# Performance work log

Hardware: AMD Instinct MI355X
Metric: run time of the kernel (lower is better)

## Reference

```python
import jax, jax.numpy as jnp
import numpy as np

B, L, D, H, W = 2, 4096, 1024, 16, 128
E = D // H

def _ln(x, g, b):
    m = jnp.mean(x, axis=-1, keepdims=True)
    v = jnp.mean((x - m) ** 2, axis=-1, keepdims=True)
    return (x - m) / jnp.sqrt(v + 1e-5) * g + b

def _swa(xn, Wqkv, bqkv, Wp, bp):
    # causal sliding-window attention: query i attends keys j in [i-W+1, i]
    b_, l_, d_ = xn.shape
    nb = l_ // W
    qkv = xn @ Wqkv + bqkv
    q, k, v = jnp.split(qkv, 3, axis=-1)
    def heads(t):
        return t.reshape(b_, l_, H, E).transpose(0, 2, 1, 3)  # [B,H,L,E]
    q, k, v = heads(q), heads(k), heads(v)
    def blk(t):
        return t.reshape(b_, H, nb, W, E)
    qb, kb, vb = blk(q), blk(k), blk(v)
    # each query block sees previous block + own block (covers the W-band)
    kprev = jnp.pad(kb, ((0, 0), (0, 0), (1, 0), (0, 0), (0, 0)))[:, :, :nb]
    vprev = jnp.pad(vb, ((0, 0), (0, 0), (1, 0), (0, 0), (0, 0)))[:, :, :nb]
    kc = jnp.concatenate([kprev, kb], axis=3)  # [B,H,nb,2W,E]
    vc = jnp.concatenate([vprev, vb], axis=3)
    scores = jnp.einsum('bhnre,bhnse->bhnrs', qb, kc) / np.float32(np.sqrt(E))
    r = jnp.arange(W)[:, None]
    s = jnp.arange(2 * W)[None, :]
    band = (s >= r + 1) & (s <= r + W)          # local coords of [i-W+1, i]
    first = band & (s >= W)                     # block 0 has no previous block
    mask = jnp.concatenate([first[None], jnp.broadcast_to(band, (nb - 1, W, 2 * W))], axis=0)
    scores = jnp.where(mask[None, None], scores, jnp.float32(-1e30))
    attn = jax.nn.softmax(scores, axis=-1)
    out = jnp.einsum('bhnrs,bhnse->bhnre', attn, vc)
    out = out.reshape(b_, H, l_, E).transpose(0, 2, 1, 3).reshape(b_, l_, d_)
    return out @ Wp + bp

def _linattn(xn, Wqkv, bqkv, Wo, bo):
    # chunked recurrent form of causal linear attention (same math as cumsum version)
    b_, l_, d_ = xn.shape
    C = 128
    nc = l_ // C
    qkv = xn @ Wqkv + bqkv
    q, k, v = jnp.split(qkv, 3, axis=-1)
    q = q.reshape(b_, l_, H, E)
    k = k.reshape(b_, l_, H, E)
    v = v.reshape(b_, l_, H, E)
    q = jax.nn.elu(q * np.float32(E ** -0.5)) + np.float32(1.0001)
    k = jax.nn.elu(k) + np.float32(1.0001)
    def chunks(t):
        return t.reshape(b_, nc, C, H, E).transpose(1, 0, 3, 2, 4)  # [nc,B,H,C,E]
    qc, kc, vc = chunks(q), chunks(k), chunks(v)
    tril = jnp.tril(jnp.ones((C, C), jnp.float32))
    def step(carry, inp):
        S, z = carry
        qi, ki, vi = inp
        A = jnp.einsum('bhce,bhde->bhcd', qi, ki) * tril
        num = jnp.einsum('bhce,bhef->bhcf', qi, S) + jnp.einsum('bhcd,bhdf->bhcf', A, vi)
        den = jnp.einsum('bhce,bhe->bhc', qi, z) + A.sum(-1)
        o = num / (den[..., None] + 1e-6)
        S = S + jnp.einsum('bhce,bhcf->bhef', ki, vi)
        z = z + ki.sum(2)
        return (S, z), o
    S0 = jnp.zeros((b_, H, E, E), jnp.float32)
    z0 = jnp.zeros((b_, H, E), jnp.float32)
    _, out = jax.lax.scan(step, (S0, z0), (qc, kc, vc))
    out = out.transpose(1, 0, 3, 2, 4).reshape(b_, l_, d_)
    return out @ Wo + bo

def setup_inputs() -> dict:
    key = jax.random.key(0)
    ks = jax.random.split(key, 9)
    def w(k, shape, s=0.02):
        return jax.random.normal(k, shape, jnp.float32) * s
    return {
        'x': jax.random.normal(ks[0], (B, L, D), jnp.float32),
        'g1': jnp.ones((D,), jnp.float32), 'b1': jnp.zeros((D,), jnp.float32),
        'Wqkv_a': w(ks[1], (D, 3 * D)), 'bqkv_a': jnp.zeros((3 * D,), jnp.float32),
        'Wp_a': w(ks[2], (D, D)), 'bp_a': jnp.zeros((D,), jnp.float32),
        'Wqkv_s': w(ks[3], (D, 3 * D)), 'bqkv_s': jnp.zeros((3 * D,), jnp.float32),
        'Wo_s': w(ks[4], (D, D)), 'bo_s': jnp.zeros((D,), jnp.float32),
        'Wo': w(ks[5], (D, D)), 'bo': jnp.zeros((D,), jnp.float32),
        'gm': jnp.ones((D,), jnp.float32), 'bm': jnp.zeros((D,), jnp.float32),
        'W1': w(ks[6], (D, 4 * D)), 'b1m': jnp.zeros((4 * D,), jnp.float32),
        'W2': w(ks[7], (4 * D, D)), 'b2m': jnp.zeros((D,), jnp.float32),
    }

def reference(x, g1, b1, Wqkv_a, bqkv_a, Wp_a, bp_a, Wqkv_s, bqkv_s, Wo_s, bo_s,
              Wo, bo, gm, bm, W1, b1m, W2, b2m):
    xn = _ln(x, g1, b1)
    attn_out = _swa(xn, Wqkv_a, bqkv_a, Wp_a, bp_a)
    ssm_out = _linattn(xn, Wqkv_s, bqkv_s, Wo_s, bo_s)
    mixed = (attn_out + ssm_out) @ Wo + bo
    x1 = x + mixed
    h = _ln(x1, gm, bm)
    mlp = jax.nn.gelu(h @ W1 + b1m, approximate=False) @ W2 + b2m
    return x1 + mlp
```

## Files before the change

### kernel.cpp

```cpp
#include <hip/hip_runtime.h>
#include <hip/hip_bf16.h>
#include <math.h>

typedef __hip_bfloat16 bf16;
typedef float f32x4 __attribute__((ext_vector_type(4)));
typedef short short8 __attribute__((ext_vector_type(8)));
typedef unsigned short u16x4 __attribute__((ext_vector_type(4)));
typedef unsigned short u16x8 __attribute__((ext_vector_type(8)));

#define AS1 __attribute__((address_space(1)))
#define AS3 __attribute__((address_space(3)))

__device__ __forceinline__ void gload16(const void* g, void* l) {
  __builtin_amdgcn_global_load_lds((const AS1 unsigned int*)g, (AS3 unsigned int*)l, 16, 0, 0);
}
__device__ __forceinline__ float b2f(unsigned short u) {
  union { unsigned int i; float f; } c; c.i = ((unsigned int)u) << 16; return c.f;
}
__device__ __forceinline__ unsigned short f2b(float f) {
  bf16 h = __float2bfloat16(f);
  unsigned short s; __builtin_memcpy(&s, &h, 2); return s;
}
__device__ __forceinline__ f32x4 mfma16(short8 a, short8 b, f32x4 c) {
  return __builtin_amdgcn_mfma_f32_16x16x32_bf16(a, b, c, 0, 0, 0);
}

#define BARR asm volatile("s_barrier" ::: "memory")
#define LGKM0 asm volatile("s_waitcnt lgkmcnt(0)" ::: "memory")
#define VM8 asm volatile("s_waitcnt vmcnt(8)" ::: "memory")
#define VM6 asm volatile("s_waitcnt vmcnt(6)" ::: "memory")
#define VM4 asm volatile("s_waitcnt vmcnt(4)" ::: "memory")
#define VM3 asm volatile("s_waitcnt vmcnt(3)" ::: "memory")
#define VM0 asm volatile("s_waitcnt vmcnt(0)" ::: "memory")
#define SB0 __builtin_amdgcn_sched_barrier(0)
#define PRIO1 __builtin_amdgcn_s_setprio(1)
#define PRIO0 __builtin_amdgcn_s_setprio(0)

__global__ __launch_bounds__(256) void ln_kernel(
    const float* __restrict__ X, const float* __restrict__ G,
    const float* __restrict__ Bb, unsigned short* __restrict__ Y) {
  __shared__ float red[8];
  const size_t row = blockIdx.x;
  const int tid = threadIdx.x;
  f32x4 v = *(const f32x4*)&X[row * 1024 + tid * 4];
  float s = 0.f, sq = 0.f;
#pragma unroll
  for (int j = 0; j < 4; ++j) { s += v[j]; sq += v[j] * v[j]; }
#pragma unroll
  for (int o = 1; o < 64; o <<= 1) { s += __shfl_xor(s, o); sq += __shfl_xor(sq, o); }
  if ((tid & 63) == 0) { red[tid >> 6] = s; red[4 + (tid >> 6)] = sq; }
  __syncthreads();
  s = red[0] + red[1] + red[2] + red[3];
  sq = red[4] + red[5] + red[6] + red[7];
  const float mean = s * (1.f / 1024.f);
  const float var = sq * (1.f / 1024.f) - mean * mean;
  const float inv = 1.f / sqrtf(var + 1e-5f);
  f32x4 gv = *(const f32x4*)&G[tid * 4];
  f32x4 bv = *(const f32x4*)&Bb[tid * 4];
  u16x4 ov;
#pragma unroll
  for (int j = 0; j < 4; ++j) ov[j] = f2b((v[j] - mean) * inv * gv[j] + bv[j]);
  *(u16x4*)&Y[row * 1024 + tid * 4] = ov;
}

struct TW7 {
  const float* S[7];
  unsigned short* D[7];
  int N[7], dld[7], doff[7], gx[7];
  int start[8];
};
__global__ __launch_bounds__(256) void transpose_w7(TW7 tw) {
  __shared__ __attribute__((aligned(16))) unsigned short t[64][72];
  const int bid = blockIdx.x;
  int c = 0;
#pragma unroll
  for (int j = 0; j < 7; ++j)
    if (bid >= tw.start[j]) c = j;
  const int local = bid - tw.start[c];
  const int k0 = (local % tw.gx[c]) * 64, n0 = (local / tw.gx[c]) * 64;
  const float* S = tw.S[c];
  unsigned short* D = tw.D[c];
  const int N = tw.N[c], dld = tw.dld[c], doff = tw.doff[c];
  const int tid = threadIdx.x;
#pragma unroll
  for (int i = 0; i < 2; ++i) {
    int cc = i * 256 + tid;
    int row = cc >> 3, c8 = cc & 7;
    f32x4 a = *(const f32x4*)&S[(size_t)(k0 + row) * N + n0 + c8 * 8];
    f32x4 b = *(const f32x4*)&S[(size_t)(k0 + row) * N + n0 + c8 * 8 + 4];
    u16x8 o;
#pragma unroll
    for (int j = 0; j < 4; ++j) { o[j] = f2b(a[j]); o[4 + j] = f2b(b[j]); }
    *(u16x8*)&t[row][c8 * 8] = o;
  }
  __syncthreads();
#pragma unroll
  for (int i = 0; i < 2; ++i) {
    int cc = i * 256 + tid;
    int nrow = cc >> 3, k8 = cc & 7;
    u16x8 o;
#pragma unroll
    for (int j = 0; j < 8; ++j) o[j] = t[k8 * 8 + j][nrow];
    *(u16x8*)&D[(size_t)(n0 + nrow) * dld + doff + k0 + k8 * 8] = o;
  }
}

__global__ __launch_bounds__(256) void bias_comb(
    const float* __restrict__ a, const float* __restrict__ b, float* __restrict__ o) {
  int i = blockIdx.x * 256 + threadIdx.x;
  o[i] = a[i] + b[i];
}

__global__ __launch_bounds__(256) void bias_cat(
    const float* __restrict__ a, const float* __restrict__ b, float* __restrict__ o, int N) {
  int i = blockIdx.x * 256 + threadIdx.x;
  o[i] = (i < N) ? a[i] : b[i - N];
}

#define EPI_STORE 0
#define EPI_GELU 1
#define EPI_RES 2

template <int EPI, int OF32>
__global__ __launch_bounds__(512, 2) void gemm_big(
    const unsigned short* __restrict__ A, const unsigned short* __restrict__ Bt,
    const float* __restrict__ bias, void* __restrict__ Cv,
    const float* __restrict__ res, int K, int ldA, int ldC) {
  __shared__ __attribute__((aligned(16))) unsigned short Abuf[2][2][16 * 512];
  __shared__ __attribute__((aligned(16))) unsigned short Bbuf[2][2][16 * 512];
  const int tid = threadIdx.x, lane = tid & 63, wv = tid >> 6;
  const int g = lane >> 4, r = lane & 15;
  const int wr = wv >> 2, wc = wv & 3;
  const size_t arow0 = (size_t)blockIdx.x * 256;
  const size_t brow0 = (size_t)blockIdx.y * 256;
  const size_t ldAs = (size_t)ldA, Ksz = (size_t)K;
  const unsigned short* gA0 = A + (arow0 + (size_t)((2 * wv + 0) * 16 + r)) * ldAs + g * 8;
  const unsigned short* gA1 = A + (arow0 + (size_t)((2 * wv + 1) * 16 + r)) * ldAs + g * 8;
  const unsigned short* gB0 = Bt + (brow0 + (size_t)((2 * wv + 0) * 16 + r)) * Ksz + g * 8;
  const unsigned short* gB1 = Bt + (brow0 + (size_t)((2 * wv + 1) * 16 + r)) * Ksz + g * 8;
  const int nT = K >> 6;
  f32x4 acc[8][4] = {};
  short8 af[8], bfr[4];

#define STG(BUF, KK, T_) do { size_t o_ = (size_t)(T_) * 64 + (KK) * 32;            \
    gload16(gA0 + o_, &Abuf[BUF][KK][(2 * wv + 0) * 512]);                           \
    gload16(gA1 + o_, &Abuf[BUF][KK][(2 * wv + 1) * 512]);                           \
    gload16(gB0 + o_, &Bbuf[BUF][KK][(2 * wv + 0) * 512]);                           \
    gload16(gB1 + o_, &Bbuf[BUF][KK][(2 * wv + 1) * 512]); } while (0)
#define RDF(CUR, KK) do {                                                            \
    _Pragma("unroll") for (int m_ = 0; m_ < 8; ++m_)                                 \
      af[m_] = *(const short8*)&Abuf[CUR][KK][(wr * 8 + m_) * 512 + lane * 8];       \
    _Pragma("unroll") for (int n_ = 0; n_ < 4; ++n_)                                 \
      bfr[n_] = *(const short8*)&Bbuf[CUR][KK][(wc * 4 + n_) * 512 + lane * 8]; } while (0)
#define MMQ() _Pragma("unroll") for (int m_ = 0; m_ < 8; ++m_)                       \
    _Pragma("unroll") for (int n_ = 0; n_ < 4; ++n_)                                 \
      acc[m_][n_] = mfma16(af[m_], bfr[n_], acc[m_][n_]);

  STG(0, 0, 0); STG(0, 1, 0); STG(1, 0, 1);
  VM8; BARR; SB0;

  for (int T = 0; T < nT; ++T) {
    const int cur = T & 1;
    RDF(cur, 0);
    if (T + 1 < nT) STG(cur ^ 1, 1, T + 1);
    BARR; LGKM0; SB0;
    PRIO1; MMQ(); PRIO0;
    if (T + 1 < nT) { VM8; } else { VM0; }
    BARR; SB0;
    RDF(cur, 1);
    if (T + 2 < nT) STG(cur, 0, T + 2);
    BARR; LGKM0; SB0;
    PRIO1; MMQ(); PRIO0;
    if (T + 2 < nT) { VM8; } else if (T + 1 < nT) { VM4; }
    BARR; SB0;
  }
#undef STG
#undef RDF
#undef MMQ

#pragma unroll
  for (int m = 0; m < 8; ++m) {
#pragma unroll
    for (int n = 0; n < 4; ++n) {
      const int col = (int)brow0 + wc * 64 + n * 16 + r;
      const float bv = bias[col];
#pragma unroll
      for (int i = 0; i < 4; ++i) {
        const size_t row = arow0 + wr * 128 + m * 16 + g * 4 + i;
        float v = acc[m][n][i] + bv;
        if (EPI == EPI_GELU) v = 0.5f * v * (1.f + erff(v * 0.70710678118f));
        if (EPI == EPI_RES) v += res[row * ldC + col];
        if (OF32) ((float*)Cv)[row * ldC + col] = v;
        else ((unsigned short*)Cv)[row * ldC + col] = f2b(v);
      }
    }
  }
}

template <int EPI, int OF32>
__global__ __launch_bounds__(512, 2) void gemm_sml(
    const unsigned short* __restrict__ A, const unsigned short* __restrict__ Bt,
    const float* __restrict__ bias, void* __restrict__ Cv,
    const float* __restrict__ res, int K, int ldA, int ldC) {
  __shared__ __attribute__((aligned(16))) unsigned short Abuf[2][2][8 * 512];
  __shared__ __attribute__((aligned(16))) unsigned short Bbuf[2][2][16 * 512];
  const int tid = threadIdx.x, lane = tid & 63, wv = tid >> 6;
  const int g = lane >> 4, r = lane & 15;
  const int wr = wv >> 2, wc = wv & 3;
  const size_t arow0 = (size_t)blockIdx.x * 128;
  const size_t brow0 = (size_t)blockIdx.y * 256;
  const size_t ldAs = (size_t)ldA, Ksz = (size_t)K;
  const unsigned short* gAs = A + (arow0 + (size_t)(wv * 16 + r)) * ldAs + g * 8;
  const unsigned short* gB0 = Bt + (brow0 + (size_t)((2 * wv + 0) * 16 + r)) * Ksz + g * 8;
  const unsigned short* gB1 = Bt + (brow0 + (size_t)((2 * wv + 1) * 16 + r)) * Ksz + g * 8;
  const int nT = K >> 6;
  f32x4 acc[4][4] = {};
  short8 af[4], bfr[4];

#define STG(BUF, KK, T_) do { size_t o_ = (size_t)(T_) * 64 + (KK) * 32;            \
    gload16(gAs + o_, &Abuf[BUF][KK][wv * 512]);                                     \
    gload16(gB0 + o_, &Bbuf[BUF][KK][(2 * wv + 0) * 512]);                           \
    gload16(gB1 + o_, &Bbuf[BUF][KK][(2 * wv + 1) * 512]); } while (0)
#define RDF(CUR, KK) do {                                                            \
    _Pragma("unroll") for (int m_ = 0; m_ < 4; ++m_)                                 \
      af[m_] = *(const short8*)&Abuf[CUR][KK][(wr * 4 + m_) * 512 + lane * 8];       \
    _Pragma("unroll") for (int n_ = 0; n_ < 4; ++n_)                                 \
      bfr[n_] = *(const short8*)&Bbuf[CUR][KK][(wc * 4 + n_) * 512 + lane * 8]; } while (0)
#define MMQ() _Pragma("unroll") for (int m_ = 0; m_ < 4; ++m_)                       \
    _Pragma("unroll") for (int n_ = 0; n_ < 4; ++n_)                                 \
      acc[m_][n_] = mfma16(af[m_], bfr[n_], acc[m_][n_]);

  STG(0, 0, 0); STG(0, 1, 0); STG(1, 0, 1);
  VM6; BARR; SB0;

  for (int T = 0; T < nT; ++T) {
    const int cur = T & 1;
    RDF(cur, 0);
    if (T + 1 < nT) STG(cur ^ 1, 1, T + 1);
    BARR; LGKM0; SB0;
    PRIO1; MMQ(); PRIO0;
    if (T + 1 < nT) { VM6; } else { VM0; }
    BARR; SB0;
    RDF(cur, 1);
    if (T + 2 < nT) STG(cur, 0, T + 2);
    BARR; LGKM0; SB0;
    PRIO1; MMQ(); PRIO0;
    if (T + 2 < nT) { VM6; } else if (T + 1 < nT) { VM3; }
    BARR; SB0;
  }
#undef STG
#undef RDF
#undef MMQ

#pragma unroll
  for (int m = 0; m < 4; ++m) {
#pragma unroll
    for (int n = 0; n < 4; ++n) {
      const int col = (int)brow0 + wc * 64 + n * 16 + r;
      const float bv = bias[col];
#pragma unroll
      for (int i = 0; i < 4; ++i) {
        const size_t row = arow0 + wr * 64 + m * 16 + g * 4 + i;
        float v = acc[m][n][i] + bv;
        if (EPI == EPI_GELU) v = 0.5f * v * (1.f + erff(v * 0.70710678118f));
        if (EPI == EPI_RES) v += res[row * ldC + col];
        if (OF32) ((float*)Cv)[row * ldC + col] = v;
        else ((unsigned short*)Cv)[row * ldC + col] = f2b(v);
      }
    }
  }
}

__global__ __launch_bounds__(256) void swa_kernel(
    const unsigned short* __restrict__ qkv, unsigned short* __restrict__ outc) {
  __shared__ __attribute__((aligned(16))) unsigned short Ks[256 * 64];
  __shared__ __attribute__((aligned(16))) unsigned short Vt[64 * 264];
  __shared__ __attribute__((aligned(16))) unsigned short Ps[128 * 264];
  __shared__ __attribute__((aligned(16))) float dn[128];
  const int bid = blockIdx.x;
  const int qb = bid & 31, h = (bid >> 5) & 15, b = bid >> 9;
  const long btok = (long)b * 4096;
  const long tok0 = btok + (long)qb * 128;
  const int tid = threadIdx.x, lane = tid & 63, wv = tid >> 6;
  const int g = lane >> 4, r = lane & 15;

#pragma unroll
  for (int i = 0; i < 8; ++i) {
    int chunk = (wv * 8 + i) * 64 + lane;
    int s = chunk >> 3, cc = (chunk & 7) ^ (s & 7);
    long kt = tok0 - 128 + s; if (kt < btok) kt = btok;
    gload16(&qkv[(size_t)kt * 6144 + 1024 + h * 64 + cc * 8], &Ks[(wv * 8 + i) * 512]);
  }
#pragma unroll
  for (int i = 0; i < 8; ++i) {
    int chunk = i * 256 + tid;
    int s = chunk >> 3, e8 = chunk & 7;
    long kt = tok0 - 128 + s; if (kt < btok) kt = btok;
    u16x8 u = *(const u16x8*)&qkv[(size_t)kt * 6144 + 2048 + h * 64 + e8 * 8];
#pragma unroll
    for (int j = 0; j < 8; ++j) Vt[(e8 * 8 + j) * 264 + s] = u[j];
  }
  short8 qf[2][2];
#pragma unroll
  for (int m = 0; m < 2; ++m)
#pragma unroll
    for (int kc = 0; kc < 2; ++kc)
      qf[m][kc] = *(const short8*)&qkv[(size_t)(tok0 + wv * 32 + m * 16 + r) * 6144 + h * 64 + kc * 32 + g * 8];
  __syncthreads();

  float rs[2][4] = {};
  for (int n = 0; n < 16; ++n) {
    const int srow = n * 16 + r;
    short8 kf0 = *(const short8*)&Ks[srow * 64 + ((g) ^ (srow & 7)) * 8];
    short8 kf1 = *(const short8*)&Ks[srow * 64 + ((4 + g) ^ (srow & 7)) * 8];
#pragma unroll
    for (int m = 0; m < 2; ++m) {
      f32x4 acc = {0.f, 0.f, 0.f, 0.f};
      acc = mfma16(qf[m][0], kf0, acc);
      acc = mfma16(qf[m][1], kf1, acc);
#pragma unroll
      for (int i = 0; i < 4; ++i) {
        int rr = wv * 32 + m * 16 + g * 4 + i;
        int ss = n * 16 + r;
        bool valid = (ss >= rr + 1) && (ss <= rr + 128) && (qb > 0 || ss >= 128);
        float p = valid ? __expf(acc[i] * 0.125f) : 0.f;
        rs[m][i] += p;
        Ps[rr * 264 + ss] = f2b(p);
      }
    }
  }
#pragma unroll
  for (int m = 0; m < 2; ++m)
#pragma unroll
    for (int i = 0; i < 4; ++i) {
      float v = rs[m][i];
      v += __shfl_xor(v, 1); v += __shfl_xor(v, 2);
      v += __shfl_xor(v, 4); v += __shfl_xor(v, 8);
      if (r == i) dn[wv * 32 + m * 16 + g * 4 + i] = v;
    }
  __syncthreads();

  f32x4 oacc[2][4] = {};
  for (int sc = 0; sc < 8; ++sc) {
    short8 pf[2], vf[4];
#pragma unroll
    for (int m = 0; m < 2; ++m)
      pf[m] = *(const short8*)&Ps[(wv * 32 + m * 16 + r) * 264 + sc * 32 + g * 8];
#pragma unroll
    for (int n = 0; n < 4; ++n)
      vf[n] = *(const short8*)&Vt[(n * 16 + r) * 264 + sc * 32 + g * 8];
#pragma unroll
    for (int m = 0; m < 2; ++m)
#pragma unroll
      for (int n = 0; n < 4; ++n)
        oacc[m][n] = mfma16(pf[m], vf[n], oacc[m][n]);
  }
#pragma unroll
  for (int m = 0; m < 2; ++m) {
    f32x4 dv = *(const f32x4*)&dn[wv * 32 + m * 16 + g * 4];
#pragma unroll
    for (int n = 0; n < 4; ++n) {
      int col = h * 64 + n * 16 + r;
#pragma unroll
      for (int i = 0; i < 4; ++i) {
        size_t row = (size_t)(tok0 + wv * 32 + m * 16 + g * 4 + i);
        outc[row * 2048 + col] = f2b(oacc[m][n][i] / dv[i]);
      }
    }
  }
}

__global__ __launch_bounds__(256) void lin_pass1(
    const unsigned short* __restrict__ qkv, float* __restrict__ KVt, float* __restrict__ kz) {
  __shared__ __attribute__((aligned(16))) unsigned short kf[128 * 72];
  __shared__ __attribute__((aligned(16))) unsigned short vs[128 * 72];
  const int bid = blockIdx.x;
  const int ch = bid & 31, h = (bid >> 5) & 15, b = bid >> 9;
  const size_t tok0 = (size_t)b * 4096 + (size_t)ch * 128;
  const int tid = threadIdx.x;
#pragma unroll
  for (int i = 0; i < 4; ++i) {
    int c = i * 256 + tid;
    int row = c >> 3, e8 = c & 7;
    u16x8 uk = *(const u16x8*)&qkv[(tok0 + row) * 6144 + 1024 + h * 64 + e8 * 8];
    u16x8 uv = *(const u16x8*)&qkv[(tok0 + row) * 6144 + 2048 + h * 64 + e8 * 8];
    u16x8 tk;
#pragma unroll
    for (int j = 0; j < 8; ++j) {
      float x = b2f(uk[j]);
      x = (x > 0.f) ? x : expm1f(x);
      tk[j] = f2b(x + 1.0001f);
    }
    *(u16x8*)&kf[row * 72 + e8 * 8] = tk;
    *(u16x8*)&vs[row * 72 + e8 * 8] = uv;
  }
  __syncthreads();
  const int e0 = (tid & 15) * 4, f0 = (tid >> 4) * 4;
  float acc[4][4] = {};
  for (int c = 0; c < 128; ++c) {
    u16x4 ku = *(const u16x4*)&kf[c * 72 + e0];
    u16x4 vu = *(const u16x4*)&vs[c * 72 + f0];
    float ke[4], vv[4];
#pragma unroll
    for (int j = 0; j < 4; ++j) { ke[j] = b2f(ku[j]); vv[j] = b2f(vu[j]); }
#pragma unroll
    for (int jf = 0; jf < 4; ++jf)
#pragma unroll
      for (int je = 0; je < 4; ++je)
        acc[jf][je] += vv[jf] * ke[je];
  }
  const size_t base = (size_t)bid * 4096;
#pragma unroll
  for (int jf = 0; jf < 4; ++jf) {
    f32x4 o = {acc[jf][0], acc[jf][1], acc[jf][2], acc[jf][3]};
    *(f32x4*)&KVt[base + (f0 + jf) * 64 + e0] = o;
  }
  if (tid < 64) {
    float s = 0.f;
    for (int c = 0; c < 128; ++c) s += b2f(kf[c * 72 + tid]);
    kz[(size_t)bid * 64 + tid] = s;
  }
}

__global__ __launch_bounds__(256) void lin_pass2(float* __restrict__ KVt, float* __restrict__ kz) {
  const int bh = blockIdx.x >> 2, sl = blockIdx.x & 3;
  const int tid = threadIdx.x;
  const size_t eo = (size_t)(sl * 256 + tid) * 4;
  f32x4 run = {0.f, 0.f, 0.f, 0.f};
  for (int ch = 0; ch < 32; ++ch) {
    float* p = &KVt[((size_t)bh * 32 + ch) * 4096 + eo];
    f32x4 c = *(f32x4*)p;
    *(f32x4*)p = run;
    run += c;
  }
  if (sl == 0 && tid < 64) {
    float rz = 0.f;
    for (int ch = 0; ch < 32; ++ch) {
      float* p = &kz[((size_t)bh * 32 + ch) * 64 + tid];
      float c = *p; *p = rz; rz += c;
    }
  }
}

__global__ __launch_bounds__(256) void lin_pass3(
    const unsigned short* __restrict__ qkv, const float* __restrict__ KVt,
    const float* __restrict__ kz, unsigned short* __restrict__ outc) {
  __shared__ __attribute__((aligned(16))) unsigned short qf[128 * 72];
  __shared__ __attribute__((aligned(16))) unsigned short kf[128 * 72];
  __shared__ __attribute__((aligned(16))) unsigned short vt[64 * 136];
  __shared__ __attribute__((aligned(16))) unsigned short st[64 * 72];
  __shared__ __attribute__((aligned(16))) unsigned short am[128 * 136];
  __shared__ __attribute__((aligned(16))) float zs[64];
  __shared__ __attribute__((aligned(16))) float dnl[128];
  const int bid = blockIdx.x;
  const int ch = bid & 31, h = (bid >> 5) & 15, b = bid >> 9;
  const size_t tok0 = (size_t)b * 4096 + (size_t)ch * 128;
  const int tid = threadIdx.x, lane = tid & 63, wv = tid >> 6;
  const int g = lane >> 4, r = lane & 15;

#pragma unroll
  for (int i = 0; i < 4; ++i) {
    int c = i * 256 + tid;
    int row = c >> 3, e8 = c & 7;
    u16x8 uq = *(const u16x8*)&qkv[(tok0 + row) * 6144 + h * 64 + e8 * 8];
    u16x8 uk = *(const u16x8*)&qkv[(tok0 + row) * 6144 + 1024 + h * 64 + e8 * 8];
    u16x8 uv = *(const u16x8*)&qkv[(tok0 + row) * 6144 + 2048 + h * 64 + e8 * 8];
    u16x8 tq, tk;
#pragma unroll
    for (int j = 0; j < 8; ++j) {
      float x = b2f(uq[j]) * 0.125f;
      x = (x > 0.f) ? x : expm1f(x);
      tq[j] = f2b(x + 1.0001f);
      float y = b2f(uk[j]);
      y = (y > 0.f) ? y : expm1f(y);
      tk[j] = f2b(y + 1.0001f);
    }
    *(u16x8*)&qf[row * 72 + e8 * 8] = tq;
    *(u16x8*)&kf[row * 72 + e8 * 8] = tk;
#pragma unroll
    for (int j = 0; j < 8; ++j) vt[(e8 * 8 + j) * 136 + row] = uv[j];
  }
#pragma unroll
  for (int i = 0; i < 2; ++i) {
    int idx = i * 256 + tid;
    int f = idx >> 3, e8 = idx & 7;
    f32x4 s0 = *(const f32x4*)&KVt[(size_t)bid * 4096 + f * 64 + e8 * 8];
    f32x4 s1 = *(const f32x4*)&KVt[(size_t)bid * 4096 + f * 64 + e8 * 8 + 4];
    u16x8 t;
#pragma unroll
    for (int j = 0; j < 4; ++j) { t[j] = f2b(s0[j]); t[4 + j] = f2b(s1[j]); }
    *(u16x8*)&st[f * 72 + e8 * 8] = t;
  }
  if (tid < 64) zs[tid] = kz[(size_t)bid * 64 + tid];
  __syncthreads();

  short8 aq[2][2];
#pragma unroll
  for (int m = 0; m < 2; ++m)
#pragma unroll
    for (int kc = 0; kc < 2; ++kc)
      aq[m][kc] = *(const short8*)&qf[(wv * 32 + m * 16 + r) * 72 + kc * 32 + g * 8];

  float rsA[2][4] = {};
  for (int n = 0; n < 8; ++n) {
    short8 bk0 = *(const short8*)&kf[(n * 16 + r) * 72 + g * 8];
    short8 bk1 = *(const short8*)&kf[(n * 16 + r) * 72 + 32 + g * 8];
#pragma unroll
    for (int m = 0; m < 2; ++m) {
      f32x4 acc = {0.f, 0.f, 0.f, 0.f};
      acc = mfma16(aq[m][0], bk0, acc);
      acc = mfma16(aq[m][1], bk1, acc);
#pragma unroll
      for (int i = 0; i < 4; ++i) {
        int rr = wv * 32 + m * 16 + g * 4 + i;
        int cc = n * 16 + r;
        float v = (cc <= rr) ? acc[i] : 0.f;
        rsA[m][i] += v;
        am[rr * 136 + cc] = f2b(v);
      }
    }
  }
#pragma unroll
  for (int m = 0; m < 2; ++m)
#pragma unroll
    for (int i = 0; i < 4; ++i) {
      float v = rsA[m][i];
      v += __shfl_xor(v, 1); v += __shfl_xor(v, 2);
      v += __shfl_xor(v, 4); v += __shfl_xor(v, 8);
      if (r == i) dnl[wv * 32 + m * 16 + g * 4 + i] = v;
    }
  __syncthreads();

  if (tid < 128) {
    float s = dnl[tid];
#pragma unroll
    for (int e = 0; e < 64; e += 4) {
      u16x4 qv = *(const u16x4*)&qf[tid * 72 + e];
      s += b2f(qv[0]) * zs[e] + b2f(qv[1]) * zs[e + 1] + b2f(qv[2]) * zs[e + 2] + b2f(qv[3]) * zs[e + 3];
    }
    dnl[tid] = s + 1e-6f;
  }

  f32x4 oac[2][4] = {};
#pragma unroll
  for (int kc = 0; kc < 2; ++kc) {
    short8 sf[4];
#pragma unroll
    for (int n = 0; n < 4; ++n) sf[n] = *(const short8*)&st[(n * 16 + r) * 72 + kc * 32 + g * 8];
#pragma unroll
    for (int m = 0; m < 2; ++m)
#pragma unroll
      for (int n = 0; n < 4; ++n)
        oac[m][n] = mfma16(aq[m][kc], sf[n], oac[m][n]);
  }
  for (int c4 = 0; c4 < 4; ++c4) {
    short8 pa[2], vb[4];
#pragma unroll
    for (int m = 0; m < 2; ++m)
      pa[m] = *(const short8*)&am[(wv * 32 + m * 16 + r) * 136 + c4 * 32 + g * 8];
#pragma unroll
    for (int n = 0; n < 4; ++n)
      vb[n] = *(const short8*)&vt[(n * 16 + r) * 136 + c4 * 32 + g * 8];
#pragma unroll
    for (int m = 0; m < 2; ++m)
#pragma unroll
      for (int n = 0; n < 4; ++n)
        oac[m][n] = mfma16(pa[m], vb[n], oac[m][n]);
  }
  __syncthreads();
#pragma unroll
  for (int m = 0; m < 2; ++m) {
    f32x4 dv = *(const f32x4*)&dnl[wv * 32 + m * 16 + g * 4];
#pragma unroll
    for (int n = 0; n < 4; ++n) {
      int col = 1024 + h * 64 + n * 16 + r;
#pragma unroll
      for (int i = 0; i < 4; ++i) {
        size_t row = tok0 + wv * 32 + m * 16 + g * 4 + i;
        outc[row * 2048 + col] = f2b(oac[m][n][i] / dv[i]);
      }
    }
  }
}

extern "C" void kernel_launch(void* const* d_in, const int* in_sizes, int n_in,
                              void* d_out, int out_size, void* d_ws, size_t ws_size,
                              hipStream_t stream) {
  (void)in_sizes; (void)n_in; (void)out_size; (void)ws_size;
  const float* x      = (const float*)d_in[0];
  const float* g1     = (const float*)d_in[1];
  const float* b1     = (const float*)d_in[2];
  const float* Wqkv_a = (const float*)d_in[3];
  const float* bqkv_a = (const float*)d_in[4];
  const float* Wp_a   = (const float*)d_in[5];
  const float* bp_a   = (const float*)d_in[6];
  const float* Wqkv_s = (const float*)d_in[7];
  const float* bqkv_s = (const float*)d_in[8];
  const float* Wo_s   = (const float*)d_in[9];
  const float* bo_s   = (const float*)d_in[10];
  const float* Wo     = (const float*)d_in[11];
  const float* bo     = (const float*)d_in[12];
  const float* gm     = (const float*)d_in[13];
  const float* bm     = (const float*)d_in[14];
  const float* W1     = (const float*)d_in[15];
  const float* b1m    = (const float*)d_in[16];
  const float* W2     = (const float*)d_in[17];
  const float* b2m    = (const float*)d_in[18];
  float* out = (float*)d_out;

  char* ws = (char*)d_ws;
  size_t off = 0;
  auto alloc = [&](size_t bytes) { char* p = ws + off; off += (bytes + 255) & ~(size_t)255; return p; };
  unsigned short* wTaS  = (unsigned short*)alloc((size_t)6144 * 1024 * 2);
  unsigned short* wTpo  = (unsigned short*)alloc((size_t)1024 * 2048 * 2);
  unsigned short* wTo   = (unsigned short*)alloc((size_t)1024 * 1024 * 2);
  unsigned short* wT1   = (unsigned short*)alloc((size_t)4096 * 1024 * 2);
  unsigned short* wT2   = (unsigned short*)alloc((size_t)1024 * 4096 * 2);
  float*          bcomb = (float*)alloc(1024 * 4);
  float*          bcat  = (float*)alloc(6144 * 4);
  unsigned short* xn    = (unsigned short*)alloc((size_t)8192 * 1024 * 2);
  unsigned short* qkvAS = (unsigned short*)alloc((size_t)8192 * 6144 * 2);
  unsigned short* comb  = (unsigned short*)alloc((size_t)8192 * 2048 * 2);
  float*          kvt   = (float*)alloc((size_t)1024 * 4096 * 4);
  float*          kzp   = (float*)alloc((size_t)1024 * 64 * 4);
  unsigned short* gbuf  = qkvAS;
  unsigned short* sum   = (unsigned short*)kvt;
  unsigned short* h_    = xn;
  float*          x1    = (float*)comb;

  TW7 tw;
  tw.S[0] = Wqkv_a; tw.D[0] = wTaS;                         tw.N[0] = 3072; tw.dld[0] = 1024; tw.doff[0] = 0;    tw.gx[0] = 16;
  tw.S[1] = Wqkv_s; tw.D[1] = wTaS + (size_t)3072 * 1024;   tw.N[1] = 3072; tw.dld[1] = 1024; tw.doff[1] = 0;    tw.gx[1] = 16;
  tw.S[2] = Wp_a;   tw.D[2] = wTpo;                         tw.N[2] = 1024; tw.dld[2] = 2048; tw.doff[2] = 0;    tw.gx[2] = 16;
  tw.S[3] = Wo_s;   tw.D[3] = wTpo;                         tw.N[3] = 1024; tw.dld[3] = 2048; tw.doff[3] = 1024; tw.gx[3] = 16;
  tw.S[4] = Wo;     tw.D[4] = wTo;                          tw.N[4] = 1024; tw.dld[4] = 1024; tw.doff[4] = 0;    tw.gx[4] = 16;
  tw.S[5] = W1;     tw.D[5] = wT1;                          tw.N[5] = 4096; tw.dld[5] = 1024; tw.doff[5] = 0;    tw.gx[5] = 16;
  tw.S[6] = W2;     tw.D[6] = wT2;                          tw.N[6] = 1024; tw.dld[6] = 4096; tw.doff[6] = 0;    tw.gx[6] = 64;
  tw.start[0] = 0;    tw.start[1] = 768;  tw.start[2] = 1536; tw.start[3] = 1792;
  tw.start[4] = 2048; tw.start[5] = 2304; tw.start[6] = 3328; tw.start[7] = 4352;
  transpose_w7<<<4352, 256, 0, stream>>>(tw);
  bias_comb<<<4, 256, 0, stream>>>(bp_a, bo_s, bcomb);
  bias_cat<<<24, 256, 0, stream>>>(bqkv_a, bqkv_s, bcat, 3072);

  ln_kernel<<<8192, 256, 0, stream>>>(x, g1, b1, xn);
  gemm_big<EPI_STORE, 0><<<dim3(32, 24), 512, 0, stream>>>(xn, wTaS, bcat, qkvAS, nullptr, 1024, 1024, 6144);
  swa_kernel<<<1024, 256, 0, stream>>>(qkvAS, comb);
  lin_pass1<<<1024, 256, 0, stream>>>(qkvAS + 3072, kvt, kzp);
  lin_pass2<<<128, 256, 0, stream>>>(kvt, kzp);
  lin_pass3<<<1024, 256, 0, stream>>>(qkvAS + 3072, kvt, kzp, comb);
  gemm_sml<EPI_STORE, 0><<<dim3(64, 4), 512, 0, stream>>>(comb, wTpo, bcomb, sum, nullptr, 2048, 2048, 1024);
  gemm_sml<EPI_RES, 1><<<dim3(64, 4), 512, 0, stream>>>(sum, wTo, bo, x1, x, 1024, 1024, 1024);
  ln_kernel<<<8192, 256, 0, stream>>>(x1, gm, bm, h_);
  gemm_big<EPI_GELU, 0><<<dim3(32, 16), 512, 0, stream>>>(h_, wT1, b1m, gbuf, nullptr, 1024, 1024, 4096);
  gemm_sml<EPI_RES, 1><<<dim3(64, 4), 512, 0, stream>>>(gbuf, wT2, b2m, out, x1, 4096, 4096, 1024);
}
```

Baseline: 589.5 us.

## Merge bias prep kernels, use fast exp ELU, parallelize kz reduction

Fuses the two tiny bias-preparation launches into one kernel, saving a launch. Replaces expm1f with __expf(x)-1 in the linear-attention ELU feature maps, giving cheaper transcendental math at some loss of accuracy near zero. Spreads the per-chunk key-sum reduction in lin_pass1 across all four waves using shared-memory partials instead of one wave serially summing 128 rows.

```diff
diff --git a/kernel.cpp b/kernel.cpp
--- a/kernel.cpp
+++ b/kernel.cpp
@@ -23,6 +23,9 @@
 }
 __device__ __forceinline__ f32x4 mfma16(short8 a, short8 b, f32x4 c) {
   return __builtin_amdgcn_mfma_f32_16x16x32_bf16(a, b, c, 0, 0, 0);
+}
+__device__ __forceinline__ float elu_fast(float x) {
+  return (x > 0.f) ? x : (__expf(x) - 1.f);
 }
 
 #define BARR asm volatile("s_barrier" ::: "memory")
@@ -105,16 +108,17 @@
   }
 }
 
-__global__ __launch_bounds__(256) void bias_comb(
-    const float* __restrict__ a, const float* __restrict__ b, float* __restrict__ o) {
+__global__ __launch_bounds__(256) void bias_prep(
+    const float* __restrict__ bp_a, const float* __restrict__ bo_s,
+    const float* __restrict__ bqkv_a, const float* __restrict__ bqkv_s,
+    float* __restrict__ bcomb, float* __restrict__ bcat) {
   int i = blockIdx.x * 256 + threadIdx.x;
-  o[i] = a[i] + b[i];
-}
-
-__global__ __launch_bounds__(256) void bias_cat(
-    const float* __restrict__ a, const float* __restrict__ b, float* __restrict__ o, int N) {
-  int i = blockIdx.x * 256 + threadIdx.x;
-  o[i] = (i < N) ? a[i] : b[i - N];
+  if (i < 1024) {
+    bcomb[i] = bp_a[i] + bo_s[i];
+  } else {
+    int j = i - 1024;
+    bcat[j] = (j < 3072) ? bqkv_a[j] : bqkv_s[j - 3072];
+  }
 }
 
 #define EPI_STORE 0
@@ -374,6 +378,7 @@
     const unsigned short* __restrict__ qkv, float* __restrict__ KVt, float* __restrict__ kz) {
   __shared__ __attribute__((aligned(16))) unsigned short kf[128 * 72];
   __shared__ __attribute__((aligned(16))) unsigned short vs[128 * 72];
+  __shared__ float kzp_s[4][64];
   const int bid = blockIdx.x;
   const int ch = bid & 31, h = (bid >> 5) & 15, b = bid >> 9;
   const size_t tok0 = (size_t)b * 4096 + (size_t)ch * 128;
@@ -387,9 +392,7 @@
     u16x8 tk;
 #pragma unroll
     for (int j = 0; j < 8; ++j) {
-      float x = b2f(uk[j]);
-      x = (x > 0.f) ? x : expm1f(x);
-      tk[j] = f2b(x + 1.0001f);
+      tk[j] = f2b(elu_fast(b2f(uk[j])) + 1.0001f);
     }
     *(u16x8*)&kf[row * 72 + e8 * 8] = tk;
     *(u16x8*)&vs[row * 72 + e8 * 8] = uv;
@@ -415,11 +418,15 @@
     f32x4 o = {acc[jf][0], acc[jf][1], acc[jf][2], acc[jf][3]};
     *(f32x4*)&KVt[base + (f0 + jf) * 64 + e0] = o;
   }
-  if (tid < 64) {
+  {
+    const int e = tid & 63, qq = tid >> 6;
     float s = 0.f;
-    for (int c = 0; c < 128; ++c) s += b2f(kf[c * 72 + tid]);
-    kz[(size_t)bid * 64 + tid] = s;
-  }
+    for (int c = qq * 32; c < qq * 32 + 32; ++c) s += b2f(kf[c * 72 + e]);
+    kzp_s[qq][e] = s;
+  }
+  __syncthreads();
+  if (tid < 64)
+    kz[(size_t)bid * 64 + tid] = kzp_s[0][tid] + kzp_s[1][tid] + kzp_s[2][tid] + kzp_s[3][tid];
 }
 
 __global__ __launch_bounds__(256) void lin_pass2(float* __restrict__ KVt, float* __restrict__ kz) {
@@ -468,12 +475,8 @@
     u16x8 tq, tk;
 #pragma unroll
     for (int j = 0; j < 8; ++j) {
-      float x = b2f(uq[j]) * 0.125f;
-      x = (x > 0.f) ? x : expm1f(x);
-      tq[j] = f2b(x + 1.0001f);
-      float y = b2f(uk[j]);
-      y = (y > 0.f) ? y : expm1f(y);
-      tk[j] = f2b(y + 1.0001f);
+      tq[j] = f2b(elu_fast(b2f(uq[j]) * 0.125f) + 1.0001f);
+      tk[j] = f2b(elu_fast(b2f(uk[j])) + 1.0001f);
     }
     *(u16x8*)&qf[row * 72 + e8 * 8] = tq;
     *(u16x8*)&kf[row * 72 + e8 * 8] = tk;
@@ -639,8 +642,7 @@
   tw.start[0] = 0;    tw.start[1] = 768;  tw.start[2] = 1536; tw.start[3] = 1792;
   tw.start[4] = 2048; tw.start[5] = 2304; tw.start[6] = 3328; tw.start[7] = 4352;
   transpose_w7<<<4352, 256, 0, stream>>>(tw);
-  bias_comb<<<4, 256, 0, stream>>>(bp_a, bo_s, bcomb);
-  bias_cat<<<24, 256, 0, stream>>>(bqkv_a, bqkv_s, bcat, 3072);
+  bias_prep<<<28, 256, 0, stream>>>(bp_a, bo_s, bqkv_a, bqkv_s, bcomb, bcat);
 
   ln_kernel<<<8192, 256, 0, stream>>>(x, g1, b1, xn);
   gemm_big<EPI_STORE, 0><<<dim3(32, 24), 512, 0, stream>>>(xn, wTaS, bcat, qkvAS, nullptr, 1024, 1024, 6144);
```

Result: faster. 566.9 us, median of 2 (-3.8%).
